# Kernel tuning notes

Measured on AMD Instinct MI355X. Metric: run time of the kernel, lower is better.

Reference implementation:

```python
import jax, jax.numpy as jnp
import numpy as np

K = 2            # negative:positive edge ratio (init arg k)
N_NODES = 4096
N_EDGES = 8192
FEAT = 64


def setup_inputs() -> dict:
    key = jax.random.key(0)
    k1, k2, k3 = jax.random.split(key, 3)
    node_feature = jax.random.normal(k1, (N_NODES, FEAT), dtype=jnp.float32)
    edge_src = jax.random.randint(k2, (N_EDGES,), 0, N_NODES, dtype=jnp.int32)
    edge_dst = jax.random.randint(k3, (N_EDGES,), 0, N_NODES, dtype=jnp.int32)
    return {"node_feature": node_feature, "edge_src": edge_src, "edge_dst": edge_dst}


def reference(node_feature, edge_src, edge_dst):
    E = edge_src.shape[0]
    N = node_feature.shape[0]
    # [E, E] pairwise mask: candidate column j is valid for row i iff
    # dst[j] != dst[i] and dst[j] != src[i]
    valid = (edge_dst[:, None] != edge_dst[None, :]) & (edge_src[:, None] != edge_dst[None, :])
    # unsorted_segment_min over rows grouped by edge_src -> [N, E]
    segmin = jax.ops.segment_min(valid.astype(jnp.int8), edge_src, num_segments=N)
    # gather back per edge -> [E, E], flatten
    m = segmin[edge_src].reshape(-1).astype(bool)  # [E*E]
    num_negatives = jnp.sum(m)
    ratio = num_negatives // E                      # integer ratio as in TF code
    keep_prob = (K / ratio).astype(jnp.float32)
    u = jax.random.uniform(jax.random.key(42), (E * E,), dtype=jnp.float32)
    keep = m & (u < keep_prob)
    # fixed-size (jit-friendly) stand-in for tf.boolean_mask: expected count is K*E;
    # pad/truncate to exactly K*E kept flat indices (fill_value=0 pads).
    idx = jnp.nonzero(keep, size=K * E, fill_value=0)[0]
    rows = idx // E
    cols = idx % E
    edge_src_neg = edge_src[rows]
    edge_dst_neg = edge_dst[cols]
    return edge_src_neg, edge_dst_neg
```

## Files before the change

### kernel.cpp

```cpp
#include <hip/hip_runtime.h>
#include <stdint.h>
#include <math.h>

typedef unsigned int u32;
typedef unsigned long long u64;

#define E_CNT   8192
#define N_CNT   4096
#define TOT_N   67108864u
#define OUT_K   16384
#define NBW     128

#define W_BAD      0
#define W_CNT_DST  524288
#define W_CNT_SRC  528384
#define W_CCOUNT   532480
#define W_SCAL     533504
#define S_NEG 0
#define S_TD  1
#define S_T9  2
#define OFF_KEEPBM 0x210000

__device__ __forceinline__ u32 rotl32(u32 x, u32 d) {
  return __builtin_amdgcn_alignbit(x, x, 32u - d);
}

__device__ __forceinline__ void threefry4_0_42(u32 i0, u32 i1, u32 i2, u32 i3, u32 o[4]) {
  const u32 k1 = 42u, k2 = 0x1BD11BF0u;
  u32 A0 = 0u, A1 = i0 + k1;
  u32 B0 = 0u, B1 = i1 + k1;
  u32 C0 = 0u, C1 = i2 + k1;
  u32 D0 = 0u, D1 = i3 + k1;
#define R4(r) { A0 += A1; B0 += B1; C0 += C1; D0 += D1; \
                A1 = rotl32(A1, r); B1 = rotl32(B1, r); C1 = rotl32(C1, r); D1 = rotl32(D1, r); \
                A1 ^= A0; B1 ^= B0; C1 ^= C0; D1 ^= D0; }
  R4(13) R4(15) R4(26) R4(6)
  A0 += k1; B0 += k1; C0 += k1; D0 += k1;
  A1 += k2 + 1u; B1 += k2 + 1u; C1 += k2 + 1u; D1 += k2 + 1u;
  R4(17) R4(29) R4(16) R4(24)
  A0 += k2; B0 += k2; C0 += k2; D0 += k2;
  A1 += 2u; B1 += 2u; C1 += 2u; D1 += 2u;
  R4(13) R4(15) R4(26) R4(6)
  A1 += k1 + 3u; B1 += k1 + 3u; C1 += k1 + 3u; D1 += k1 + 3u;
  R4(17) R4(29) R4(16) R4(24)
  A0 += k1; B0 += k1; C0 += k1; D0 += k1;
  A1 += k2 + 4u; B1 += k2 + 4u; C1 += k2 + 4u; D1 += k2 + 4u;
  R4(13) R4(15) R4(26) R4(6)
  A0 += k2; B0 += k2; C0 += k2; D0 += k2;
  A1 += 5u; B1 += 5u; C1 += 5u; D1 += 5u;
#undef R4
  o[0] = A0 ^ A1; o[1] = B0 ^ B1; o[2] = C0 ^ C1; o[3] = D0 ^ D1;
}

__global__ void k_init(const int* __restrict__ src, const int* __restrict__ dst,
                       u32* __restrict__ ws32, int* __restrict__ out) {
  const u32 b = blockIdx.x, t = threadIdx.x;
  if (b == 0) {
    __shared__ u32 hs[N_CNT], hd[N_CNT];
#pragma unroll
    for (int k = 0; k < 16; ++k) { hs[t + 256 * k] = 0; hd[t + 256 * k] = 0; }
    __syncthreads();
#pragma unroll
    for (int k = 0; k < 32; ++k) {
      u32 e = t + 256u * (u32)k;
      atomicAdd(&hs[(u32)src[e]], 1u);
      atomicAdd(&hd[(u32)dst[e]], 1u);
    }
    __syncthreads();
#pragma unroll
    for (int k = 0; k < 16; ++k) {
      u32 n = t + 256 * k;
      ws32[W_CNT_SRC + n] = hs[n];
      ws32[W_CNT_DST + n] = hd[n];
    }
    if (t < 8) ws32[W_SCAL + t] = 0;
    return;
  }
  if (b == 1 && t < 8) ws32[W_SCAL + t] = 0;
  u32 g = (b - 1) * 256u + t;
  if (g < 524288u) {
    u32 row = g >> 7, cw = g & 127u;
    ws32[W_BAD + g] = (cw == (row >> 5)) ? (1u << (row & 31u)) : 0u;
  } else if (g < 525312u) {
    ws32[W_CCOUNT + (g - 524288u)] = 0u;
  } else {
    u32 r = g - 525312u;
    out[r] = (r < OUT_K) ? src[0] : dst[0];
  }
}

__global__ void k_build(const int* __restrict__ src, const int* __restrict__ dst,
                        u32* __restrict__ ws32) {
  u32* bad     = ws32 + W_BAD;
  const u32* cs = ws32 + W_CNT_SRC;
  const u32* cd = ws32 + W_CNT_DST;
  u32* scal    = ws32 + W_SCAL;
  const u32 b = blockIdx.x, t = threadIdx.x;
  const u32 wv = t >> 6, ln = t & 63u;
  __shared__ u32 red[4];

  u32 e = b * 256u + t;
  u32 s = (u32)src[e], d = (u32)dst[e];
  u32 bit = 1u << (d & 31u);
  u32 old = atomicOr(&bad[s * NBW + (d >> 5)], bit);
  u32 acc = (!(old & bit)) ? cs[s] * cd[d] : 0u;
  if (t < 128u) {
    u32 n = b * 128u + t;
    acc += cs[n] * cd[n];
  }
#pragma unroll
  for (int off = 32; off > 0; off >>= 1) acc += __shfl_down(acc, off, 64);
  if (ln == 0) red[wv] = acc;
  __syncthreads();
  if (t == 0) {
    atomicAdd(&scal[S_NEG], red[0] + red[1] + red[2] + red[3]);
    __threadfence();
    if (atomicAdd(&scal[S_TD], 1u) == 31u) {
      u32 nn = TOT_N - atomicAdd(&scal[S_NEG], 0u);
      u32 ratio = nn >> 13;
      float kp = 2.0f / (float)ratio;
      u32 T = (u32)ceil((double)kp * 8388608.0);
      u32 T9 = (T >= (1u << 23)) ? 0xFFFFFFFFu : (T << 9);
      atomicExch(&scal[S_T9], T9);
    }
  }
}

__global__ void __launch_bounds__(256, 8) k_sample(const int* __restrict__ src,
                                                   const int* __restrict__ dst,
                                                   const u32* __restrict__ ws32,
                                                   u64* __restrict__ keep_bm,
                                                   u32* __restrict__ ccount) {
  const u32* bad = ws32 + W_BAD;
  const u32 T9 = ws32[W_SCAL + S_T9];
  const u32 wv = threadIdx.x >> 6, ln = threadIdx.x & 63u;
  const u32 i0w = blockIdx.x * 2048u + wv * 512u;
  u64 words[8]; u64 any = 0;
#pragma unroll
  for (int j = 0; j < 2; ++j) {
    u32 o[4];
    u32 ia = i0w + (u32)j * 256u + ln;
    threefry4_0_42(ia, ia + 64u, ia + 128u, ia + 192u, o);
#pragma unroll
    for (int m = 0; m < 4; ++m) {
      words[4 * j + m] = __ballot(o[m] < T9);
      any |= words[4 * j + m];
    }
  }
  if (any) {
#pragma unroll
    for (int k = 0; k < 8; ++k) {
      if (words[k]) {
        u32 i = i0w + (u32)k * 64u + ln;
        bool kp2 = (words[k] >> ln) & 1ull;
        if (kp2) {
          u32 n = (u32)src[i >> 13], v = (u32)dst[i & 8191u];
          kp2 = ((bad[n * NBW + (v >> 5)] >> (v & 31u)) & 1u) == 0u;
        }
        words[k] = __ballot(kp2);
      }
    }
  }
  if (ln == 0) {
    ulonglong2* p = (ulonglong2*)&keep_bm[i0w >> 6];
    p[0] = make_ulonglong2(words[0], words[1]);
    p[1] = make_ulonglong2(words[2], words[3]);
    p[2] = make_ulonglong2(words[4], words[5]);
    p[3] = make_ulonglong2(words[6], words[7]);
    u32 c = 0;
#pragma unroll
    for (int k = 0; k < 8; ++k) c += (u32)__popcll(words[k]);
    if (c) atomicAdd(&ccount[i0w >> 16], c);
  }
}

__device__ __forceinline__ u32 wave_iscan(u32 v, u32 ln) {
#pragma unroll
  for (int off = 1; off < 64; off <<= 1) {
    u32 n = __shfl_up(v, off, 64);
    if (ln >= (u32)off) v += n;
  }
  return v;
}

__global__ void k_compact(const int* __restrict__ src, const int* __restrict__ dst,
                          const u64* __restrict__ keep_bm, const u32* __restrict__ ccount,
                          int* __restrict__ out) {
  const u32 c = blockIdx.x, t = threadIdx.x;
  const u32 wv = t >> 6, ln = t & 63u;
  __shared__ u32 wtot[4], wtot2[4];
  __shared__ u32 base_sh;

  u32 v0 = ccount[4 * t], v1 = ccount[4 * t + 1], v2 = ccount[4 * t + 2], v3 = ccount[4 * t + 3];
  u32 s4 = v0 + v1 + v2 + v3;
  u32 is = wave_iscan(s4, ln);
  if (ln == 63) wtot[wv] = is;
  __syncthreads();
  u32 wpre = 0;
#pragma unroll
  for (int w = 0; w < 4; ++w) if ((u32)w < wv) wpre += wtot[w];
  if (t == (c >> 2)) {
    u32 excl = (is + wpre) - s4;
    if ((c & 3u) > 0) excl += v0;
    if ((c & 3u) > 1) excl += v1;
    if ((c & 3u) > 2) excl += v2;
    base_sh = excl;
  }
  __syncthreads();
  u32 rank0 = base_sh;

  const u64* wp = keep_bm + (size_t)c * 1024u;
  u64 w[4]; u32 cnt = 0;
#pragma unroll
  for (int k = 0; k < 4; ++k) { w[k] = wp[4 * t + k]; cnt += (u32)__popcll(w[k]); }
  u32 is2 = wave_iscan(cnt, ln);
  if (ln == 63) wtot2[wv] = is2;
  __syncthreads();
  u32 wpre2 = 0;
#pragma unroll
  for (int ww = 0; ww < 4; ++ww) if ((u32)ww < wv) wpre2 += wtot2[ww];
  u32 rank = rank0 + (is2 + wpre2) - cnt;
  u32 tb = (c << 16) + (t << 8);
#pragma unroll
  for (int k = 0; k < 4; ++k) {
    u64 bits = w[k];
    while (bits) {
      int bb = __ffsll((unsigned long long)bits) - 1;
      if (rank < OUT_K) {
        u32 tt = tb + (u32)k * 64u + (u32)bb;
        out[rank]         = src[tt >> 13];
        out[OUT_K + rank] = dst[tt & 8191u];
      }
      rank++;
      bits &= bits - 1;
    }
  }
}

extern "C" void kernel_launch(void* const* d_in, const int* in_sizes, int n_in,
                              void* d_out, int out_size, void* d_ws, size_t ws_size,
                              hipStream_t stream) {
  const int* src = (const int*)d_in[1];
  const int* dst = (const int*)d_in[2];
  int* out = (int*)d_out;
  u32* ws32 = (u32*)d_ws;
  u64* keep_bm = (u64*)((char*)d_ws + OFF_KEEPBM);
  u32* ccount = ws32 + W_CCOUNT;

  k_init<<<2181, 256, 0, stream>>>(src, dst, ws32, out);
  k_build<<<32, 256, 0, stream>>>(src, dst, ws32);
  k_sample<<<TOT_N / 2048, 256, 0, stream>>>(src, dst, ws32, keep_bm, ccount);
  k_compact<<<1024, 256, 0, stream>>>(src, dst, keep_bm, ccount, out);
}
```

Before: 193.5 us.

## Fuse init and build into one per-row-slice kernel using shared-memory bitmaps

```diff
diff --git a/kernel.cpp b/kernel.cpp
--- a/kernel.cpp
+++ b/kernel.cpp
@@ -12,14 +12,14 @@
 #define NBW     128
 
 #define W_BAD      0
-#define W_CNT_DST  524288
-#define W_CNT_SRC  528384
 #define W_CCOUNT   532480
 #define W_SCAL     533504
 #define S_NEG 0
 #define S_TD  1
 #define S_T9  2
 #define OFF_KEEPBM 0x210000
+
+#define BLD_NB 128
 
 __device__ __forceinline__ u32 rotl32(u32 x, u32 d) {
   return __builtin_amdgcn_alignbit(x, x, 32u - d);
@@ -52,71 +52,71 @@
   o[0] = A0 ^ A1; o[1] = B0 ^ B1; o[2] = C0 ^ C1; o[3] = D0 ^ D1;
 }
 
-__global__ void k_init(const int* __restrict__ src, const int* __restrict__ dst,
-                       u32* __restrict__ ws32, int* __restrict__ out) {
-  const u32 b = blockIdx.x, t = threadIdx.x;
-  if (b == 0) {
-    __shared__ u32 hs[N_CNT], hd[N_CNT];
-#pragma unroll
-    for (int k = 0; k < 16; ++k) { hs[t + 256 * k] = 0; hd[t + 256 * k] = 0; }
-    __syncthreads();
-#pragma unroll
-    for (int k = 0; k < 32; ++k) {
-      u32 e = t + 256u * (u32)k;
-      atomicAdd(&hs[(u32)src[e]], 1u);
-      atomicAdd(&hd[(u32)dst[e]], 1u);
-    }
-    __syncthreads();
-#pragma unroll
-    for (int k = 0; k < 16; ++k) {
-      u32 n = t + 256 * k;
-      ws32[W_CNT_SRC + n] = hs[n];
-      ws32[W_CNT_DST + n] = hd[n];
-    }
-    if (t < 8) ws32[W_SCAL + t] = 0;
-    return;
-  }
-  if (b == 1 && t < 8) ws32[W_SCAL + t] = 0;
-  u32 g = (b - 1) * 256u + t;
-  if (g < 524288u) {
-    u32 row = g >> 7, cw = g & 127u;
-    ws32[W_BAD + g] = (cw == (row >> 5)) ? (1u << (row & 31u)) : 0u;
-  } else if (g < 525312u) {
-    ws32[W_CCOUNT + (g - 524288u)] = 0u;
-  } else {
-    u32 r = g - 525312u;
-    out[r] = (r < OUT_K) ? src[0] : dst[0];
-  }
-}
-
-__global__ void k_build(const int* __restrict__ src, const int* __restrict__ dst,
-                        u32* __restrict__ ws32) {
-  u32* bad     = ws32 + W_BAD;
-  const u32* cs = ws32 + W_CNT_SRC;
-  const u32* cd = ws32 + W_CNT_DST;
-  u32* scal    = ws32 + W_SCAL;
+__global__ void __launch_bounds__(256) k_build(const int* __restrict__ src,
+                                               const int* __restrict__ dst,
+                                               u32* __restrict__ ws32,
+                                               int* __restrict__ out) {
+  __shared__ u32 bm[32 * NBW];
+  __shared__ u32 hs[N_CNT];
+  __shared__ u32 hd[N_CNT];
+  __shared__ u32 red[4];
+  u32* ccount = ws32 + W_CCOUNT;
+  u32* scal   = ws32 + W_SCAL;
   const u32 b = blockIdx.x, t = threadIdx.x;
   const u32 wv = t >> 6, ln = t & 63u;
-  __shared__ u32 red[4];
-
-  u32 e = b * 256u + t;
-  u32 s = (u32)src[e], d = (u32)dst[e];
-  u32 bit = 1u << (d & 31u);
-  u32 old = atomicOr(&bad[s * NBW + (d >> 5)], bit);
-  u32 acc = (!(old & bit)) ? cs[s] * cd[d] : 0u;
-  if (t < 128u) {
-    u32 n = b * 128u + t;
-    acc += cs[n] * cd[n];
-  }
-#pragma unroll
-  for (int off = 32; off > 0; off >>= 1) acc += __shfl_down(acc, off, 64);
+  const u32 rowlo = b * 32u;
+
+#pragma unroll
+  for (int k = 0; k < 16; ++k) {
+    hs[t + 256 * k] = 0; hd[t + 256 * k] = 0; bm[t + 256 * k] = 0;
+  }
+  __syncthreads();
+#pragma unroll
+  for (int k = 0; k < 32; ++k) {
+    u32 e = t + 256u * (u32)k;
+    u32 s = (u32)src[e], d = (u32)dst[e];
+    atomicAdd(&hs[s], 1u);
+    atomicAdd(&hd[d], 1u);
+    if ((s >> 5) == b) atomicOr(&bm[(s - rowlo) * NBW + (d >> 5)], 1u << (d & 31u));
+  }
+  if (t < 32u) {
+    u32 n = rowlo + t;
+    atomicOr(&bm[t * NBW + (n >> 5)], 1u << (n & 31u));
+  }
+  __syncthreads();
+
+  u32 acc = 0;
+  for (int r = (int)wv; r < 32; r += 4) {
+    u32 n = rowlo + (u32)r;
+    u32 sum = 0;
+#pragma unroll
+    for (int h = 0; h < 2; ++h) {
+      u32 w = ln + 64u * (u32)h;
+      u32 bits = bm[r * NBW + w];
+      while (bits) { int bb = __ffs(bits) - 1; sum += hd[(w << 5) + (u32)bb]; bits &= bits - 1; }
+    }
+#pragma unroll
+    for (int off = 32; off > 0; off >>= 1) sum += __shfl_down(sum, off, 64);
+    if (ln == 0) acc += hs[n] * ((u32)E_CNT - sum);
+  }
   if (ln == 0) red[wv] = acc;
+
+  uint4* gslice = (uint4*)(ws32 + W_BAD + b * 4096u);
+#pragma unroll
+  for (int k = 0; k < 4; ++k) {
+    u32 w0 = 1024u * (u32)k + 4u * t;
+    gslice[256 * k + t] = make_uint4(bm[w0], bm[w0 + 1], bm[w0 + 2], bm[w0 + 3]);
+  }
+  if (t < 8u) ccount[b * 8u + t] = 0u;
+  u32 oi = b * 256u + t;
+  out[oi] = (oi < OUT_K) ? src[0] : dst[0];
+
   __syncthreads();
   if (t == 0) {
     atomicAdd(&scal[S_NEG], red[0] + red[1] + red[2] + red[3]);
     __threadfence();
-    if (atomicAdd(&scal[S_TD], 1u) == 31u) {
-      u32 nn = TOT_N - atomicAdd(&scal[S_NEG], 0u);
+    if (atomicAdd(&scal[S_TD], 1u) == (u32)(BLD_NB - 1)) {
+      u32 nn = atomicAdd(&scal[S_NEG], 0u);
       u32 ratio = nn >> 13;
       float kp = 2.0f / (float)ratio;
       u32 T = (u32)ceil((double)kp * 8388608.0);
@@ -247,8 +247,8 @@
   u64* keep_bm = (u64*)((char*)d_ws + OFF_KEEPBM);
   u32* ccount = ws32 + W_CCOUNT;
 
-  k_init<<<2181, 256, 0, stream>>>(src, dst, ws32, out);
-  k_build<<<32, 256, 0, stream>>>(src, dst, ws32);
+  hipMemsetAsync((char*)d_ws + (size_t)W_SCAL * 4, 0, 8, stream);
+  k_build<<<BLD_NB, 256, 0, stream>>>(src, dst, ws32, out);
   k_sample<<<TOT_N / 2048, 256, 0, stream>>>(src, dst, ws32, keep_bm, ccount);
   k_compact<<<1024, 256, 0, stream>>>(src, dst, keep_bm, ccount, out);
 }
```

Result: no change. 192.2 us (-0.7%).
